# Kernel optimization log

Hardware: AMD Instinct MI355X
Metric: run time of the kernel (lower is better)

Reference implementation:

```python
import jax, jax.numpy as jnp
import numpy as np

T, B, IN, H, OUT = 128, 1024, 47, 646, 5

def setup_inputs() -> dict:
    key = jax.random.key(0)
    ks = jax.random.split(key, 11)
    s_in = 1.0 / np.sqrt(H)
    return {
        "xs": jax.random.normal(ks[0], (T, B, IN), dtype=jnp.float32),
        "W_ih0": jax.random.normal(ks[1], (H, IN), dtype=jnp.float32) * s_in,
        "W_hh0": jax.random.normal(ks[2], (H, H), dtype=jnp.float32) * s_in,
        "b_ih0": jax.random.normal(ks[3], (H,), dtype=jnp.float32) * s_in,
        "b_hh0": jax.random.normal(ks[4], (H,), dtype=jnp.float32) * s_in,
        "W_ih1": jax.random.normal(ks[5], (H, H), dtype=jnp.float32) * s_in,
        "W_hh1": jax.random.normal(ks[6], (H, H), dtype=jnp.float32) * s_in,
        "b_ih1": jax.random.normal(ks[7], (H,), dtype=jnp.float32) * s_in,
        "b_hh1": jax.random.normal(ks[8], (H,), dtype=jnp.float32) * s_in,
        "W_out": jax.random.normal(ks[9], (OUT, H), dtype=jnp.float32) * s_in,
        "b_out": jnp.zeros((OUT,), dtype=jnp.float32),
    }

def reference(xs, W_ih0, W_hh0, b_ih0, b_hh0, W_ih1, W_hh1, b_ih1, b_hh1, W_out, b_out):
    batch = xs.shape[1]
    h0 = jnp.zeros((batch, H), dtype=xs.dtype)
    h1 = jnp.zeros((batch, H), dtype=xs.dtype)

    def step(carry, x_t):
        h0, h1 = carry
        # layer 0: Elman cell, tanh
        h0 = jnp.tanh(x_t @ W_ih0.T + b_ih0 + h0 @ W_hh0.T + b_hh0)
        # layer 1 consumes layer 0's output at this timestep
        h1 = jnp.tanh(h0 @ W_ih1.T + b_ih1 + h1 @ W_hh1.T + b_hh1)
        return (h0, h1), None

    (h0, h1), _ = jax.lax.scan(step, (h0, h1), xs)
    # classifier on last layer's final hidden state
    logits = h1 @ W_out.T + b_out  # [B, 5]
    return logits
```

## Files before the change

kernel.cpp:

```cpp
#include <hip/hip_runtime.h>
#include <hip/hip_bf16.h>

#define T_STEPS 128
#define B_SZ    1024
#define IN_SZ   47
#define H_SZ    646
#define OUT_SZ  5

#define XK    96
#define K0    768
#define K1    1344
#define N0PAD 704
#define N1PAD 672
#define RING  17
#define SLAB  172032
#define FSTR  160

#define NL0B  7
#define NL1B  14
#define NBLK  (8 * (NL0B + NL1B))

typedef __hip_bfloat16 bf16;
typedef unsigned short ush;
using frag8 = __attribute__((ext_vector_type(8))) short;
using f32x4 = __attribute__((ext_vector_type(4))) float;


__global__ void prep_xs(const float* __restrict__ xs, bf16* __restrict__ xs_pad) {
    int idx = blockIdx.x * blockDim.x + threadIdx.x;
    if (idx >= T_STEPS * B_SZ * XK) return;
    int k = idx % XK;
    int rb = idx / XK;
    float v = (k < IN_SZ) ? xs[(size_t)rb * IN_SZ + k] : 0.f;
    xs_pad[idx] = __float2bfloat16(v);
}

__global__ void pack_w0(const float* __restrict__ Wih, const float* __restrict__ Whh,
                        bf16* __restrict__ Wc) {
    int idx = blockIdx.x * blockDim.x + threadIdx.x;
    if (idx >= N0PAD * K0) return;
    int j = idx / K0, k = idx % K0;
    float v = 0.f;
    if (j < H_SZ) {
        if (k < IN_SZ)                      v = Wih[(size_t)j * IN_SZ + k];
        else if (k >= XK && k < XK + H_SZ)  v = Whh[(size_t)j * H_SZ + (k - XK)];
    }
    Wc[idx] = __float2bfloat16(v);
}

__global__ void pack_w1(const float* __restrict__ Wih, const float* __restrict__ Whh,
                        bf16* __restrict__ Wc) {
    int idx = blockIdx.x * blockDim.x + threadIdx.x;
    if (idx >= N1PAD * K1) return;
    int j = idx / K1, k = idx % K1;
    float v = 0.f;
    if (j < H_SZ) {
        if (k < H_SZ)                          v = Wih[(size_t)j * H_SZ + k];
        else if (k >= 672 && k < 672 + H_SZ)   v = Whh[(size_t)j * H_SZ + (k - 672)];
    }
    Wc[idx] = __float2bfloat16(v);
}

__global__ void pack_bias(const float* __restrict__ bi, const float* __restrict__ bh,
                          float* __restrict__ b, int n) {
    int j = blockIdx.x * blockDim.x + threadIdx.x;
    if (j >= n) return;
    b[j] = (j < H_SZ) ? (bi[j] + bh[j]) : 0.f;
}


__device__ __forceinline__ void tanh_store(ush* dst, float x) {
    x = fminf(fmaxf(x, -15.f), 15.f);
    float e = __expf(2.f * x);
    bf16 hb = __float2bfloat16((e - 1.f) / (e + 1.f));
    *dst = *(ush*)&hb;
}

__device__ __forceinline__ void poll_ge(int* p, int need) {
    while (__hip_atomic_load(p, __ATOMIC_RELAXED, __HIP_MEMORY_SCOPE_AGENT) < need)
        __builtin_amdgcn_s_sleep(16);
}

__global__ __launch_bounds__(512, 2) void persist(
    const bf16* __restrict__ xs_pad, const bf16* __restrict__ Wc0,
    const bf16* __restrict__ Wc1, const float* __restrict__ b0,
    const float* __restrict__ b1, bf16* __restrict__ Sring,
    int* __restrict__ flags)
{
    extern __shared__ ush Wlds[];
    const int bid  = blockIdx.x;
    const int rg   = bid & 7;
    const int c8   = bid >> 3;
    const bool isL0 = (c8 < NL0B);
    const int tid  = threadIdx.x;
    const int wv   = tid >> 6;
    const int lane = tid & 63;
    const int q8   = (lane >> 4) * 8;
    const int l15  = lane & 15;

    if (isL0) {
        const int col0 = c8 * 96;
        for (int g = wv; g < 144; g += 8) {
            int kc = g / 6, ct = g % 6;
            const bf16* src = Wc0 + (size_t)(col0 + ct*16 + l15) * K0 + kc*32 + q8;
            *(uint4*)&Wlds[g*512 + lane*8] = *(const uint4*)src;
        }
    } else {
        const int col0 = (c8 - NL0B) * 48;
        for (int g = wv; g < 126; g += 8) {
            int kc = g / 3, ct = g % 3;
            const bf16* src = Wc1 + (size_t)(col0 + ct*16 + l15) * K1 + kc*32 + q8;
            *(uint4*)&Wlds[g*512 + lane*8] = *(const uint4*)src;
        }
    }
    __syncthreads();

    const int loc = wv * 16 + l15;
    bf16* const ringbase = Sring + (size_t)rg * RING * SLAB;
    int*  const fL0 = flags + rg * FSTR;
    int*  const fL1 = flags + (8 + rg) * FSTR;

    if (isL0) {
        const int col0 = c8 * 96;
        float bias[6];
        #pragma unroll
        for (int ct = 0; ct < 6; ++ct) bias[ct] = b0[col0 + ct*16 + l15];

        for (int p = 0; p < 128; ++p) {
            if (tid == 0) {
                if (p > 0)   poll_ge(&fL0[p-1], NL0B);
                if (p >= 17) poll_ge(&fL1[p-16], NL1B);
            }
            __syncthreads();
            if (p >= RING + 1 && (p - 1) % RING == 0)
                __builtin_amdgcn_fence(__ATOMIC_ACQUIRE, "agent");
            const bf16* rsl = ringbase + (size_t)((p + RING - 1) % RING) * SLAB;
            bf16*       wsl = ringbase + (size_t)(p % RING) * SLAB;

            const bf16* xr = xs_pad + ((size_t)p * B_SZ + rg*128 + loc) * XK + q8;
            const bf16* hr = rsl + (size_t)loc * K1 + q8;
            uint4 abuf[24];
            #pragma unroll
            for (int i = 0; i < 24; ++i)
                abuf[i] = (i < 3) ? *(const uint4*)(xr + i*32)
                                  : *(const uint4*)(hr + (i-3)*32);
            f32x4 acc[6] = {};
            #pragma unroll
            for (int kc = 0; kc < 24; ++kc) {
                frag8 af = *(const frag8*)&abuf[kc];
                #pragma unroll
                for (int ct = 0; ct < 6; ++ct) {
                    frag8 wf = *(const frag8*)&Wlds[(kc*6+ct)*512 + lane*8];
                    acc[ct] = __builtin_amdgcn_mfma_f32_16x16x32_bf16(
                        af, wf, acc[ct], 0, 0, 0);
                }
            }
            const int rbase = wv*16 + (lane>>4)*4;
            #pragma unroll
            for (int ct = 0; ct < 6; ++ct) {
                const int col = col0 + ct*16 + l15;
                if (col < H_SZ) {
                    #pragma unroll
                    for (int i = 0; i < 4; ++i)
                        tanh_store((ush*)(wsl + (size_t)(rbase+i)*K1 + col),
                                   acc[ct][i] + bias[ct]);
                }
            }
            __syncthreads();
            if (tid == 0)
                __hip_atomic_fetch_add(&fL0[p], 1, __ATOMIC_RELAXED,
                                       __HIP_MEMORY_SCOPE_AGENT);
        }
    } else {
        const int col0 = (c8 - NL0B) * 48;
        float bias[3];
        #pragma unroll
        for (int ct = 0; ct < 3; ++ct) bias[ct] = b1[col0 + ct*16 + l15];

        for (int q = 1; q <= 128; ++q) {
            if (tid == 0) {
                poll_ge(&fL0[q-1], NL0B);
                if (q > 1) poll_ge(&fL1[q-1], NL1B);
            }
            __syncthreads();
            if (q >= RING + 1 && (q - 1) % RING == 0)
                __builtin_amdgcn_fence(__ATOMIC_ACQUIRE, "agent");
            const bf16* rsl = ringbase + (size_t)((q + RING - 1) % RING) * SLAB;
            bf16*       wsl = ringbase + (size_t)(q % RING) * SLAB;

            const bf16* ar = rsl + (size_t)loc * K1 + q8;
            uint4 abuf[42];
            #pragma unroll
            for (int i = 0; i < 42; ++i) abuf[i] = *(const uint4*)(ar + i*32);
            f32x4 acc[3] = {};
            #pragma unroll
            for (int kc = 0; kc < 42; ++kc) {
                frag8 af = *(const frag8*)&abuf[kc];
                #pragma unroll
                for (int ct = 0; ct < 3; ++ct) {
                    frag8 wf = *(const frag8*)&Wlds[(kc*3+ct)*512 + lane*8];
                    acc[ct] = __builtin_amdgcn_mfma_f32_16x16x32_bf16(
                        af, wf, acc[ct], 0, 0, 0);
                }
            }
            const int rbase = wv*16 + (lane>>4)*4;
            #pragma unroll
            for (int ct = 0; ct < 3; ++ct) {
                const int col = col0 + ct*16 + l15;
                if (col < H_SZ) {
                    #pragma unroll
                    for (int i = 0; i < 4; ++i)
                        tanh_store((ush*)(wsl + (size_t)(rbase+i)*K1 + 672 + col),
                                   acc[ct][i] + bias[ct]);
                }
            }
            __syncthreads();
            if (tid == 0)
                __hip_atomic_fetch_add(&fL1[q], 1, __ATOMIC_RELAXED,
                                       __HIP_MEMORY_SCOPE_AGENT);
        }
    }
}

__global__ __launch_bounds__(256) void classifier(
    const bf16* __restrict__ Sring, const float* __restrict__ Wout,
    const float* __restrict__ bout, float* __restrict__ out)
{
    const int wave = threadIdx.x >> 6, lane = threadIdx.x & 63;
    const int row = blockIdx.x * 4 + wave;
    const int rg = row >> 7, loc = row & 127;
    const bf16* h1 = Sring + ((size_t)rg * RING + (128 % RING)) * SLAB
                     + (size_t)loc * K1 + 672;
    float acc[OUT_SZ] = {0.f, 0.f, 0.f, 0.f, 0.f};
    for (int k = lane; k < H_SZ; k += 64) {
        float h = __bfloat162float(h1[k]);
        #pragma unroll
        for (int o = 0; o < OUT_SZ; ++o) acc[o] += h * Wout[(size_t)o * H_SZ + k];
    }
    #pragma unroll
    for (int o = 0; o < OUT_SZ; ++o) {
        float v = acc[o];
        #pragma unroll
        for (int off = 32; off; off >>= 1) v += __shfl_down(v, off, 64);
        if (lane == 0) out[(size_t)row * OUT_SZ + o] = v + bout[o];
    }
}


extern "C" void kernel_launch(void* const* d_in, const int* in_sizes, int n_in,
                              void* d_out, int out_size, void* d_ws, size_t ws_size,
                              hipStream_t stream) {
    const float* xs   = (const float*)d_in[0];
    const float* Wih0 = (const float*)d_in[1];
    const float* Whh0 = (const float*)d_in[2];
    const float* bih0 = (const float*)d_in[3];
    const float* bhh0 = (const float*)d_in[4];
    const float* Wih1 = (const float*)d_in[5];
    const float* Whh1 = (const float*)d_in[6];
    const float* bih1 = (const float*)d_in[7];
    const float* bhh1 = (const float*)d_in[8];
    const float* Wout = (const float*)d_in[9];
    const float* bout = (const float*)d_in[10];
    float* out = (float*)d_out;

    char* ws = (char*)d_ws;
    size_t off = 0;
    bf16* xs_pad = (bf16*)(ws + off); off += (size_t)T_STEPS * B_SZ * XK * 2;
    bf16* Wc0    = (bf16*)(ws + off); off += (size_t)N0PAD * K0 * 2;
    bf16* Wc1    = (bf16*)(ws + off); off += (size_t)N1PAD * K1 * 2;
    float* b0    = (float*)(ws + off); off += (size_t)N0PAD * 4;
    float* b1    = (float*)(ws + off); off += (size_t)N1PAD * 4;
    bf16* Sring  = (bf16*)(ws + off); off += (size_t)8 * RING * SLAB * 2;
    int*  flags  = (int*)(ws + off);  off += (size_t)16 * FSTR * 4;

    hipMemsetAsync(Sring, 0, (size_t)8 * RING * SLAB * 2, stream);
    hipMemsetAsync(flags, 0, (size_t)16 * FSTR * 4, stream);

    prep_xs <<<(T_STEPS * B_SZ * XK + 255) / 256, 256, 0, stream>>>(xs, xs_pad);
    pack_w0 <<<(N0PAD * K0 + 255) / 256, 256, 0, stream>>>(Wih0, Whh0, Wc0);
    pack_w1 <<<(N1PAD * K1 + 255) / 256, 256, 0, stream>>>(Wih1, Whh1, Wc1);
    pack_bias<<<(N0PAD + 255) / 256, 256, 0, stream>>>(bih0, bhh0, b0, N0PAD);
    pack_bias<<<(N1PAD + 255) / 256, 256, 0, stream>>>(bih1, bhh1, b1, N1PAD);

    hipFuncSetAttribute((const void*)persist,
                        hipFuncAttributeMaxDynamicSharedMemorySize, 147456);
    void* args[] = { (void*)&xs_pad, (void*)&Wc0, (void*)&Wc1, (void*)&b0,
                     (void*)&b1, (void*)&Sring, (void*)&flags };
    hipLaunchCooperativeKernel((const void*)persist, dim3(NBLK), dim3(512),
                               args, 147456, stream);

    classifier<<<B_SZ / 4, 256, 0, stream>>>(Sring, Wout, bout, out);
}
```

Before: 1.645 ms.

## Split layer-1 wait so h0 half runs before h1 flag, prefetch x early

Layer-1 blocks now wait only for the layer-0 flag, compute the h0 half of the K reduction, and only then wait for the layer-1 flag before loading and multiplying the h1 half. Layer-0 blocks issue their x-input loads before polling the flag. The spin-wait sleep is shortened so waiters react to flag changes sooner. Together these are meant to shorten the critical path of the cross-block dependency chain, at the cost of an extra barrier per step and more polling traffic.

```diff
diff --git a/kernel.cpp b/kernel.cpp
--- a/kernel.cpp
+++ b/kernel.cpp
@@ -78,7 +78,7 @@
 
 __device__ __forceinline__ void poll_ge(int* p, int need) {
     while (__hip_atomic_load(p, __ATOMIC_RELAXED, __HIP_MEMORY_SCOPE_AGENT) < need)
-        __builtin_amdgcn_s_sleep(16);
+        __builtin_amdgcn_s_sleep(2);
 }
 
 __global__ __launch_bounds__(512, 2) void persist(
@@ -127,6 +127,14 @@
         for (int ct = 0; ct < 6; ++ct) bias[ct] = b0[col0 + ct*16 + l15];
 
         for (int p = 0; p < 128; ++p) {
+            const bf16* rsl = ringbase + (size_t)((p + RING - 1) % RING) * SLAB;
+            bf16*       wsl = ringbase + (size_t)(p % RING) * SLAB;
+
+            const bf16* xr = xs_pad + ((size_t)p * B_SZ + rg*128 + loc) * XK + q8;
+            uint4 xbuf[3];
+            #pragma unroll
+            for (int i = 0; i < 3; ++i) xbuf[i] = *(const uint4*)(xr + i*32);
+
             if (tid == 0) {
                 if (p > 0)   poll_ge(&fL0[p-1], NL0B);
                 if (p >= 17) poll_ge(&fL1[p-16], NL1B);
@@ -134,20 +142,17 @@
             __syncthreads();
             if (p >= RING + 1 && (p - 1) % RING == 0)
                 __builtin_amdgcn_fence(__ATOMIC_ACQUIRE, "agent");
-            const bf16* rsl = ringbase + (size_t)((p + RING - 1) % RING) * SLAB;
-            bf16*       wsl = ringbase + (size_t)(p % RING) * SLAB;
-
-            const bf16* xr = xs_pad + ((size_t)p * B_SZ + rg*128 + loc) * XK + q8;
+
             const bf16* hr = rsl + (size_t)loc * K1 + q8;
-            uint4 abuf[24];
-            #pragma unroll
-            for (int i = 0; i < 24; ++i)
-                abuf[i] = (i < 3) ? *(const uint4*)(xr + i*32)
-                                  : *(const uint4*)(hr + (i-3)*32);
+            uint4 hbuf[21];
+            #pragma unroll
+            for (int i = 0; i < 21; ++i) hbuf[i] = *(const uint4*)(hr + i*32);
+
             f32x4 acc[6] = {};
             #pragma unroll
             for (int kc = 0; kc < 24; ++kc) {
-                frag8 af = *(const frag8*)&abuf[kc];
+                frag8 af = (kc < 3) ? *(const frag8*)&xbuf[kc]
+                                    : *(const frag8*)&hbuf[kc-3];
                 #pragma unroll
                 for (int ct = 0; ct < 6; ++ct) {
                     frag8 wf = *(const frag8*)&Wlds[(kc*6+ct)*512 + lane*8];
@@ -178,24 +183,41 @@
         for (int ct = 0; ct < 3; ++ct) bias[ct] = b1[col0 + ct*16 + l15];
 
         for (int q = 1; q <= 128; ++q) {
-            if (tid == 0) {
-                poll_ge(&fL0[q-1], NL0B);
-                if (q > 1) poll_ge(&fL1[q-1], NL1B);
-            }
+            const bf16* rsl = ringbase + (size_t)((q + RING - 1) % RING) * SLAB;
+            bf16*       wsl = ringbase + (size_t)(q % RING) * SLAB;
+            const bf16* ar  = rsl + (size_t)loc * K1 + q8;
+
+            if (tid == 0) poll_ge(&fL0[q-1], NL0B);
             __syncthreads();
             if (q >= RING + 1 && (q - 1) % RING == 0)
                 __builtin_amdgcn_fence(__ATOMIC_ACQUIRE, "agent");
-            const bf16* rsl = ringbase + (size_t)((q + RING - 1) % RING) * SLAB;
-            bf16*       wsl = ringbase + (size_t)(q % RING) * SLAB;
-
-            const bf16* ar = rsl + (size_t)loc * K1 + q8;
-            uint4 abuf[42];
-            #pragma unroll
-            for (int i = 0; i < 42; ++i) abuf[i] = *(const uint4*)(ar + i*32);
+
+            uint4 h0buf[21];
+            #pragma unroll
+            for (int i = 0; i < 21; ++i) h0buf[i] = *(const uint4*)(ar + i*32);
             f32x4 acc[3] = {};
             #pragma unroll
-            for (int kc = 0; kc < 42; ++kc) {
-                frag8 af = *(const frag8*)&abuf[kc];
+            for (int kc = 0; kc < 21; ++kc) {
+                frag8 af = *(const frag8*)&h0buf[kc];
+                #pragma unroll
+                for (int ct = 0; ct < 3; ++ct) {
+                    frag8 wf = *(const frag8*)&Wlds[(kc*3+ct)*512 + lane*8];
+                    acc[ct] = __builtin_amdgcn_mfma_f32_16x16x32_bf16(
+                        af, wf, acc[ct], 0, 0, 0);
+                }
+            }
+
+            if (q > 1) {
+                if (tid == 0) poll_ge(&fL1[q-1], NL1B);
+                __syncthreads();
+            }
+            uint4 h1buf[21];
+            #pragma unroll
+            for (int i = 0; i < 21; ++i)
+                h1buf[i] = *(const uint4*)(ar + (21 + i)*32);
+            #pragma unroll
+            for (int kc = 21; kc < 42; ++kc) {
+                frag8 af = *(const frag8*)&h1buf[kc-21];
                 #pragma unroll
                 for (int ct = 0; ct < 3; ++ct) {
                     frag8 wf = *(const frag8*)&Wlds[(kc*3+ct)*512 + lane*8];
```

After: 1.620 ms. No clear change (-1.5%).
